# Kernel optimization log

Measured on AMD Instinct MI355X. Metric: run time of the kernel, lower is better.

## Reference

```python
import jax, jax.numpy as jnp
import numpy as np
import math

B, T, C, H = 2, 2048, 1024, 16
HD = C // H  # head_dim = 64
SCALE = 1.0 / math.sqrt(HD)


def _e8_head_dirs(n_heads: int) -> np.ndarray:
    # Type-1 E8 roots in original generation order: (+-1 at i, +-1 at j), i<j,
    # sign order (-1,-1),(-1,1),(1,-1),(1,1); then L2-normalized (norm sqrt(2)).
    roots = []
    for i in range(8):
        for j in range(i + 1, 8):
            for si in (-1.0, 1.0):
                for sj in (-1.0, 1.0):
                    r = np.zeros(8, dtype=np.float32)
                    r[i] = si
                    r[j] = sj
                    roots.append(r)
    roots = np.stack(roots)  # [112, 8], first n_heads used
    roots = roots / np.linalg.norm(roots, axis=1, keepdims=True)
    return roots[:n_heads]


def setup_inputs() -> dict:
    key = jax.random.key(0)
    k1, k2, k3, k4 = jax.random.split(key, 4)
    x = jax.random.normal(k1, (B, T, C), dtype=jnp.float32)
    # nn.Linear-style init scale
    w_qkv = jax.random.normal(k2, (C, 3 * C), dtype=jnp.float32) * (1.0 / math.sqrt(C))
    w_out = jax.random.normal(k3, (C, C), dtype=jnp.float32) * (1.0 / math.sqrt(C))
    head_scales = jax.random.normal(k4, (H,), dtype=jnp.float32) * 0.1
    head_dirs = jnp.asarray(_e8_head_dirs(H))  # [H, 8] buffer (not trained)
    return {"x": x, "w_qkv": w_qkv, "w_out": w_out,
            "head_scales": head_scales, "head_dirs": head_dirs}


def reference(x, w_qkv, w_out, head_scales, head_dirs):
    Bx, Tx, Cx = x.shape
    qkv = (x @ w_qkv).reshape(Bx, Tx, 3, H, HD)
    qkv = jnp.transpose(qkv, (2, 0, 3, 1, 4))  # [3, B, H, T, HD]
    q, k, v = qkv[0], qkv[1], qkv[2]
    scores = jnp.einsum('bhqd,bhkd->bhqk', q, k) * SCALE  # [B,H,T,T]
    causal = jnp.tril(jnp.ones((Tx, Tx), dtype=bool))
    scores = jnp.where(causal[None, None], scores, -jnp.inf)
    # E8 geometric bias: rank-1 per-head bias from projections onto root dirs
    q_proj = jnp.einsum('bhtd,hd->bht', q[..., :8], head_dirs)
    k_proj = jnp.einsum('bhtd,hd->bht', k[..., :8], head_dirs)
    geo_bias = q_proj[..., :, None] * k_proj[..., None, :]  # [B,H,T,T]
    scores = scores + head_scales[None, :, None, None] * geo_bias
    attn = jax.nn.softmax(scores, axis=-1)
    out = jnp.einsum('bhqk,bhkd->bhqd', attn, v)  # [B,H,T,HD]
    out = jnp.transpose(out, (0, 2, 1, 3)).reshape(Bx, Tx, Cx)
    return out @ w_out
```

## Files before the change

kernel.cpp:

```cpp
#include <hip/hip_runtime.h>
#include <stdint.h>


typedef float f32x4 __attribute__((ext_vector_type(4)));
typedef unsigned short u16x8 __attribute__((ext_vector_type(8)));
typedef unsigned short u16x4 __attribute__((ext_vector_type(4)));
typedef unsigned int u32x2 __attribute__((ext_vector_type(2)));
typedef __bf16 bf16x8 __attribute__((ext_vector_type(8)));

static __device__ __forceinline__ unsigned short f2bf(float f) {
  unsigned u = __float_as_uint(f);
  u += 0x7FFFu + ((u >> 16) & 1u);
  return (unsigned short)(u >> 16);
}
static __device__ __forceinline__ float bf2f(unsigned short s) {
  return __uint_as_float(((unsigned)s) << 16);
}
static __device__ __forceinline__ f32x4 mfma16(u16x8 a, u16x8 b, f32x4 c) {
  return __builtin_amdgcn_mfma_f32_16x16x32_bf16(
      __builtin_bit_cast(bf16x8, a), __builtin_bit_cast(bf16x8, b), c, 0, 0, 0);
}
static __device__ __forceinline__ unsigned cvtpk(float lo, float hi) {
  unsigned d;
  asm("v_cvt_pk_bf16_f32 %0, %1, %2" : "=v"(d) : "v"(lo), "v"(hi));
  return d;
}

#define GLD16(gp, lp) __builtin_amdgcn_global_load_lds( \
    (const __attribute__((address_space(1))) unsigned int*)(gp), \
    (__attribute__((address_space(3))) unsigned int*)(lp), 16, 0, 0)

__global__ __launch_bounds__(256) void k_prep(const float* __restrict__ x,
                                              const float* __restrict__ wqkv,
                                              const float* __restrict__ wout,
                                              unsigned short* __restrict__ xb,
                                              unsigned short* __restrict__ wqkvT,
                                              unsigned short* __restrict__ woutT) {
  __shared__ float t[64][65];
  const int bid = blockIdx.x;
  if (bid < 4096) {
    int i = bid * 256 + threadIdx.x;
    f32x4 v = *(const f32x4*)(x + (size_t)i * 4);
    u16x4 o;
#pragma unroll
    for (int j = 0; j < 4; ++j) o[j] = f2bf(v[j]);
    *(u16x4*)(xb + (size_t)i * 4) = o;
    return;
  }
  const float* in;
  unsigned short* out;
  int Cc, bx, by;
  if (bid < 4864) {
    int tt = bid - 4096;
    in = wqkv; out = wqkvT; Cc = 3072;
    bx = tt % 48; by = tt / 48;
  } else {
    int tt = bid - 4864;
    in = wout; out = woutT; Cc = 1024;
    bx = tt & 15; by = tt >> 4;
  }
  const int R = 1024;
  int tr = by * 64, tc = bx * 64;
  int tx = threadIdx.x & 15, ty = threadIdx.x >> 4;
#pragma unroll
  for (int i = 0; i < 4; ++i) {
    int rr = ty + i * 16;
    f32x4 v = *(const f32x4*)(in + (size_t)(tr + rr) * Cc + tc + tx * 4);
#pragma unroll
    for (int j = 0; j < 4; ++j) t[rr][tx * 4 + j] = v[j];
  }
  __syncthreads();
#pragma unroll
  for (int i = 0; i < 4; ++i) {
    int cc = ty + i * 16;
    int rr = tx * 4;
    u16x4 o;
#pragma unroll
    for (int j = 0; j < 4; ++j) o[j] = f2bf(t[rr + j][cc]);
    *(u16x4*)(out + (size_t)(tc + cc) * R + tr + rr) = o;
  }
}

template <int MODE>
__global__ __launch_bounds__(256) void k_gemm(const unsigned short* __restrict__ A,
                                              const unsigned short* __restrict__ Bt,
                                              unsigned short* __restrict__ qo,
                                              unsigned short* __restrict__ ko,
                                              unsigned short* __restrict__ vTo,
                                              float* __restrict__ fo) {
  __shared__ unsigned short lA[128 * 32];
  __shared__ unsigned short lB[128 * 32];
  const int tid = threadIdx.x;
  const int lane = tid & 63, wid = tid >> 6;
  const int wr = wid >> 1, wc = wid & 1;
  const int r = lane & 15, g = lane >> 4;
  const int mbase = blockIdx.y * 128;
  const int nbase = blockIdx.x * 128;

  f32x4 acc[4][4] = {};

  for (int kt = 0; kt < 32; ++kt) {
    __syncthreads();
#pragma unroll
    for (int p = 0; p < 2; ++p) {
      int L = p * 4096 + tid * 16;
      int row = L >> 6;
      int blk = (L >> 4) & 3;
      GLD16(A + (size_t)(mbase + row) * 1024 + kt * 32 + blk * 8, lA + (L >> 1));
      GLD16(Bt + (size_t)(nbase + row) * 1024 + kt * 32 + blk * 8, lB + (L >> 1));
    }
    __syncthreads();
    u16x8 af[4], bfv[4];
#pragma unroll
    for (int m = 0; m < 4; ++m)
      af[m] = *(const u16x8*)(lA + (wr * 64 + m * 16 + r) * 32 + g * 8);
#pragma unroll
    for (int n = 0; n < 4; ++n)
      bfv[n] = *(const u16x8*)(lB + (wc * 64 + n * 16 + r) * 32 + g * 8);
#pragma unroll
    for (int m = 0; m < 4; ++m)
#pragma unroll
      for (int n = 0; n < 4; ++n) acc[m][n] = mfma16(af[m], bfv[n], acc[m][n]);
  }

#pragma unroll
  for (int m = 0; m < 4; ++m) {
#pragma unroll
    for (int n = 0; n < 4; ++n) {
      int ng = nbase + wc * 64 + n * 16 + r;
      int m0 = mbase + wr * 64 + m * 16 + g * 4;
      if (MODE == 0) {
        int sec = ng >> 10, rem = ng & 1023, hh = rem >> 6, d = rem & 63;
        int b = m0 >> 11, t0 = m0 & 2047;
        size_t bh = (size_t)(b * 16 + hh);
        if (sec == 2) {
          u16x4 o;
#pragma unroll
          for (int e = 0; e < 4; ++e) o[e] = f2bf(acc[m][n][e]);
          *(u16x4*)(vTo + (bh * 64 + d) * 2048 + t0) = o;
        } else {
          unsigned short* dst = (sec == 0 ? qo : ko);
#pragma unroll
          for (int e = 0; e < 4; ++e)
            dst[(bh * 2048 + t0 + e) * 64 + d] = f2bf(acc[m][n][e]);
        }
      } else {
#pragma unroll
        for (int e = 0; e < 4; ++e)
          fo[(size_t)(m0 + e) * 1024 + ng] = acc[m][n][e];
      }
    }
  }
}

__global__ __launch_bounds__(256) void k_attn(const unsigned short* __restrict__ qb,
                                              const unsigned short* __restrict__ kb,
                                              const unsigned short* __restrict__ vTb,
                                              const float* __restrict__ hsc,
                                              const float* __restrict__ hdir,
                                              unsigned short* __restrict__ o2) {
  __shared__ unsigned short lK[2][64 * 64];
  __shared__ unsigned short lV[2][64 * 64];
  __shared__ unsigned short lP[4][16 * 64];

  const int tid = threadIdx.x, lane = tid & 63, wid = tid >> 6;
  const int r = lane & 15, g = lane >> 4;
  const int bid = blockIdx.x;
  const int u = bid & 255, kq = bid >> 8;
  const int bh = u & 31, j = u >> 5;
  const int a = (kq == 0) ? j : (kq == 1) ? (31 - j) : (kq == 2) ? (8 + j) : (23 - j);
  const int nk = a + 1;
  const int qbase = a * 64;
  const int h = bh & 15, bi = bh >> 4;

  const size_t kbase = (size_t)bh * (2048 * 64);
  const size_t vbase = (size_t)bh * (64 * 2048);

  auto STAGE = [&](int buf, int kt) {
    unsigned short* dK = (unsigned short*)lK[buf];
    unsigned short* dV = (unsigned short*)lV[buf];
#pragma unroll
    for (int p = 0; p < 2; ++p) {
      int L = p * 4096 + tid * 16;
      int row = L >> 7;
      int cb = (L >> 4) & 7;
      int cbg = cb ^ (row & 7);
      GLD16(kb + kbase + (size_t)(kt * 64 + row) * 64 + cbg * 8, dK + (L >> 1));
      GLD16(vTb + vbase + (size_t)row * 2048 + kt * 64 + cbg * 8, dV + (L >> 1));
    }
  };

  STAGE(0, 0);

  const float LOG2E = 1.44269504088896f;
  const float hs = hsc[h];
  float dir8[8];
#pragma unroll
  for (int j2 = 0; j2 < 8; ++j2) dir8[j2] = hdir[h * 8 + j2];

  u16x8 qc0, qc1;
  {
    const unsigned short* qrow = qb + ((size_t)bh * 2048 + qbase + wid * 16 + r) * 64;
    float proj = 0.f;
    u16x8 qv = *(const u16x8*)qrow;
#pragma unroll
    for (int j2 = 0; j2 < 8; ++j2) proj += bf2f(qv[j2]) * dir8[j2];
#pragma unroll
    for (int s = 0; s < 2; ++s) {
      u16x8 raw = *(const u16x8*)(qrow + s * 32 + g * 8);
      u16x8 ov;
#pragma unroll
      for (int j2 = 0; j2 < 8; ++j2) {
        float v = bf2f(raw[j2]) * (0.125f * LOG2E);
        if (s == 0 && g == 0) v += (hs * LOG2E) * proj * dir8[j2];
        ov[j2] = f2bf(v);
      }
      if (s == 0) qc0 = ov; else qc1 = ov;
    }
  }

  f32x4 accO[4] = {};
  float lp = 0.f;
  unsigned short* pw = &lP[wid][0];
  const int swz = (r & 7) << 4;
  const int qq = qbase + wid * 16 + r;

  asm volatile("s_waitcnt vmcnt(0)" ::: "memory");
  __builtin_amdgcn_sched_barrier(0);
  __builtin_amdgcn_s_barrier();

  for (int kt = 0; kt < nk; ++kt) {
    if (kt + 1 < nk) STAGE((kt + 1) & 1, kt + 1);

    const char* lKc = (const char*)lK[kt & 1];
    const char* lVc = (const char*)lV[kt & 1];

    f32x4 accS[4];
    __builtin_amdgcn_s_setprio(1);
#pragma unroll
    for (int ct = 0; ct < 4; ++ct) {
      f32x4 s4 = {0.f, 0.f, 0.f, 0.f};
      int krow = ct * 16 + r;
      int sw = (krow & 7) << 4;
      u16x8 kf0 = *(const u16x8*)(lKc + krow * 128 + ((g * 16) ^ sw));
      u16x8 kf1 = *(const u16x8*)(lKc + krow * 128 + ((64 + g * 16) ^ sw));
      s4 = mfma16(kf0, qc0, s4);
      s4 = mfma16(kf1, qc1, s4);
      accS[ct] = s4;
    }
    __builtin_amdgcn_s_setprio(0);

    if (kt == nk - 1) {
#pragma unroll
      for (int ct = 0; ct < 4; ++ct)
#pragma unroll
        for (int e = 0; e < 4; ++e) {
          int kk = kt * 64 + ct * 16 + g * 4 + e;
          if (kk > qq) accS[ct][e] = -1e30f;
        }
    }

    float p[4][4];
#pragma unroll
    for (int ct = 0; ct < 4; ++ct)
#pragma unroll
      for (int e = 0; e < 4; ++e) p[ct][e] = exp2f(accS[ct][e]);
#pragma unroll
    for (int ct = 0; ct < 4; ++ct)
      lp += (p[ct][0] + p[ct][1]) + (p[ct][2] + p[ct][3]);

#pragma unroll
    for (int ct = 0; ct < 4; ++ct) {
      u32x2 w;
      w[0] = cvtpk(p[ct][0], p[ct][1]);
      w[1] = cvtpk(p[ct][2], p[ct][3]);
      *(u32x2*)((char*)pw + r * 128 + ((ct * 32 + g * 8) ^ swz)) = w;
    }
    asm volatile("s_waitcnt lgkmcnt(0)" ::: "memory");
    __builtin_amdgcn_sched_barrier(0);

    __builtin_amdgcn_s_setprio(1);
#pragma unroll
    for (int s = 0; s < 2; ++s) {
      u16x8 pa = *(const u16x8*)((const char*)pw + r * 128 + ((s * 64 + g * 16) ^ swz));
#pragma unroll
      for (int dt = 0; dt < 4; ++dt) {
        int dd = dt * 16 + r;
        u16x8 vf = *(const u16x8*)(lVc + dd * 128 + ((s * 64 + g * 16) ^ ((dd & 7) << 4)));
        accO[dt] = mfma16(vf, pa, accO[dt]);
      }
    }
    __builtin_amdgcn_s_setprio(0);

    if (kt + 1 < nk) {
      asm volatile("s_waitcnt vmcnt(0)" ::: "memory");
      __builtin_amdgcn_sched_barrier(0);
      __builtin_amdgcn_s_barrier();
    }
  }

  lp += __shfl_xor(lp, 16, 64);
  lp += __shfl_xor(lp, 32, 64);
  float inv = 1.f / lp;
#pragma unroll
  for (int dt = 0; dt < 4; ++dt) {
    u16x4 o;
#pragma unroll
    for (int e = 0; e < 4; ++e) o[e] = f2bf(accO[dt][e] * inv);
    *(u16x4*)(o2 + ((size_t)(bi * 2048 + qq)) * 1024 + h * 64 + dt * 16 + g * 4) = o;
  }
}

extern "C" void kernel_launch(void* const* d_in, const int* in_sizes, int n_in,
                              void* d_out, int out_size, void* d_ws, size_t ws_size,
                              hipStream_t stream) {
  const float* x    = (const float*)d_in[0];
  const float* wqkv = (const float*)d_in[1];
  const float* wout = (const float*)d_in[2];
  const float* hsc  = (const float*)d_in[3];
  const float* hdir = (const float*)d_in[4];
  float* outp = (float*)d_out;

  char* ws = (char*)d_ws;
  unsigned short* xb    = (unsigned short*)(ws + 0);
  unsigned short* wqkvT = (unsigned short*)(ws + 8388608);
  unsigned short* woutT = (unsigned short*)(ws + 14680064);
  unsigned short* qb    = (unsigned short*)(ws + 16777216);
  unsigned short* kb    = (unsigned short*)(ws + 25165824);
  unsigned short* vT    = (unsigned short*)(ws + 33554432);
  unsigned short* x2b   = (unsigned short*)(ws + 41943040);
  if (ws_size < 50331648u) return;

  k_prep<<<5120, 256, 0, stream>>>(x, wqkv, wout, xb, wqkvT, woutT);
  k_gemm<0><<<dim3(24, 32), 256, 0, stream>>>(xb, wqkvT, qb, kb, vT, nullptr);
  k_attn<<<dim3(1024), 256, 0, stream>>>(qb, kb, vT, hsc, hdir, x2b);
  k_gemm<1><<<dim3(8, 32), 256, 0, stream>>>(x2b, woutT, nullptr, nullptr, nullptr, outp);
}
```

Measured before the change: 111.2 us.

## Pair causal query tiles per block and split key tile across wave halves

The attention kernel now launches 512-thread blocks. Each block handles two query tiles, a short one and its mirrored long one (pr and 31-pr), so every block does exactly 33 key-tile iterations. Within a block, two groups of four waves each take half of each 64-key tile, and their partial outputs and row sums are merged through LDS at the diagonal tile. This balances the causal workload and halves the per-wave MFMA work per key tile. In exchange it adds a cross-wave reduction with an extra barrier and higher register and LDS pressure.

```diff
diff --git a/kernel.cpp b/kernel.cpp
--- a/kernel.cpp
+++ b/kernel.cpp
@@ -153,41 +153,39 @@
   }
 }
 
-__global__ __launch_bounds__(256) void k_attn(const unsigned short* __restrict__ qb,
-                                              const unsigned short* __restrict__ kb,
-                                              const unsigned short* __restrict__ vTb,
-                                              const float* __restrict__ hsc,
-                                              const float* __restrict__ hdir,
-                                              unsigned short* __restrict__ o2) {
+__global__ __launch_bounds__(512, 4) void k_attn(const unsigned short* __restrict__ qb,
+                                                 const unsigned short* __restrict__ kb,
+                                                 const unsigned short* __restrict__ vTb,
+                                                 const float* __restrict__ hsc,
+                                                 const float* __restrict__ hdir,
+                                                 unsigned short* __restrict__ o2) {
   __shared__ unsigned short lK[2][64 * 64];
   __shared__ unsigned short lV[2][64 * 64];
-  __shared__ unsigned short lP[4][16 * 64];
+  __shared__ unsigned short lP[8][16 * 64];
+  __shared__ float lL[128];
 
   const int tid = threadIdx.x, lane = tid & 63, wid = tid >> 6;
   const int r = lane & 15, g = lane >> 4;
+  const int qw = wid & 3, kh = wid >> 2;
   const int bid = blockIdx.x;
-  const int u = bid & 255, kq = bid >> 8;
-  const int bh = u & 31, j = u >> 5;
-  const int a = (kq == 0) ? j : (kq == 1) ? (31 - j) : (kq == 2) ? (8 + j) : (23 - j);
-  const int nk = a + 1;
-  const int qbase = a * 64;
+  const int bh = bid & 31;
+  const int pr = bid >> 5;
+  const int tA = pr, tB = 31 - pr;
+  const int nkA = pr + 1;
   const int h = bh & 15, bi = bh >> 4;
 
   const size_t kbase = (size_t)bh * (2048 * 64);
   const size_t vbase = (size_t)bh * (64 * 2048);
 
   auto STAGE = [&](int buf, int kt) {
-    unsigned short* dK = (unsigned short*)lK[buf];
-    unsigned short* dV = (unsigned short*)lV[buf];
-#pragma unroll
-    for (int p = 0; p < 2; ++p) {
-      int L = p * 4096 + tid * 16;
-      int row = L >> 7;
-      int cb = (L >> 4) & 7;
-      int cbg = cb ^ (row & 7);
-      GLD16(kb + kbase + (size_t)(kt * 64 + row) * 64 + cbg * 8, dK + (L >> 1));
-      GLD16(vTb + vbase + (size_t)row * 2048 + kt * 64 + cbg * 8, dV + (L >> 1));
-    }
+    int L = tid * 16;
+    int row = L >> 7;
+    int cb = (L >> 4) & 7;
+    int cbg = cb ^ (row & 7);
+    GLD16(kb + kbase + (size_t)(kt * 64 + row) * 64 + cbg * 8,
+          (unsigned short*)lK[buf] + (L >> 1));
+    GLD16(vTb + vbase + (size_t)row * 2048 + kt * 64 + cbg * 8,
+          (unsigned short*)lV[buf] + (L >> 1));
   };
 
   STAGE(0, 0);
@@ -198,9 +196,9 @@
 #pragma unroll
   for (int j2 = 0; j2 < 8; ++j2) dir8[j2] = hdir[h * 8 + j2];
 
-  u16x8 qc0, qc1;
-  {
-    const unsigned short* qrow = qb + ((size_t)bh * 2048 + qbase + wid * 16 + r) * 64;
+  u16x8 qAc0, qAc1, qBc0, qBc1;
+  auto QF = [&](int rowbase, u16x8& c0, u16x8& c1) {
+    const unsigned short* qrow = qb + ((size_t)bh * 2048 + rowbase + r) * 64;
     float proj = 0.f;
     u16x8 qv = *(const u16x8*)qrow;
 #pragma unroll
@@ -215,99 +213,126 @@
         if (s == 0 && g == 0) v += (hs * LOG2E) * proj * dir8[j2];
         ov[j2] = f2bf(v);
       }
-      if (s == 0) qc0 = ov; else qc1 = ov;
-    }
-  }
+      if (s == 0) c0 = ov; else c1 = ov;
+    }
+  };
+  QF(tA * 64 + qw * 16, qAc0, qAc1);
+  QF(tB * 64 + qw * 16, qBc0, qBc1);
 
   f32x4 accO[4] = {};
   float lp = 0.f;
+  u16x8 qc0 = qAc0, qc1 = qAc1;
+  int qq = tA * 64 + qw * 16 + r;
   unsigned short* pw = &lP[wid][0];
   const int swz = (r & 7) << 4;
-  const int qq = qbase + wid * 16 + r;
 
   asm volatile("s_waitcnt vmcnt(0)" ::: "memory");
   __builtin_amdgcn_sched_barrier(0);
   __builtin_amdgcn_s_barrier();
 
-  for (int kt = 0; kt < nk; ++kt) {
-    if (kt + 1 < nk) STAGE((kt + 1) & 1, kt + 1);
-
-    const char* lKc = (const char*)lK[kt & 1];
-    const char* lVc = (const char*)lV[kt & 1];
-
-    f32x4 accS[4];
+  for (int it = 0; it < 33; ++it) {
+    if (it + 1 < 33) {
+      int nt = it + 1;
+      STAGE(nt & 1, (nt < nkA) ? nt : nt - nkA);
+    }
+    const int kt = (it < nkA) ? it : it - nkA;
+    const char* lKc = (const char*)lK[it & 1];
+    const char* lVc = (const char*)lV[it & 1];
+
+    f32x4 accS[2];
     __builtin_amdgcn_s_setprio(1);
 #pragma unroll
-    for (int ct = 0; ct < 4; ++ct) {
-      f32x4 s4 = {0.f, 0.f, 0.f, 0.f};
-      int krow = ct * 16 + r;
+    for (int cl = 0; cl < 2; ++cl) {
+      int krow = (kh * 2 + cl) * 16 + r;
       int sw = (krow & 7) << 4;
       u16x8 kf0 = *(const u16x8*)(lKc + krow * 128 + ((g * 16) ^ sw));
       u16x8 kf1 = *(const u16x8*)(lKc + krow * 128 + ((64 + g * 16) ^ sw));
+      f32x4 s4 = {0.f, 0.f, 0.f, 0.f};
       s4 = mfma16(kf0, qc0, s4);
       s4 = mfma16(kf1, qc1, s4);
-      accS[ct] = s4;
+      accS[cl] = s4;
     }
     __builtin_amdgcn_s_setprio(0);
 
-    if (kt == nk - 1) {
-#pragma unroll
-      for (int ct = 0; ct < 4; ++ct)
+    const bool diag = (it == nkA - 1) || (it == 32);
+    if (diag) {
+#pragma unroll
+      for (int cl = 0; cl < 2; ++cl)
 #pragma unroll
         for (int e = 0; e < 4; ++e) {
-          int kk = kt * 64 + ct * 16 + g * 4 + e;
-          if (kk > qq) accS[ct][e] = -1e30f;
+          int kk = kt * 64 + (kh * 2 + cl) * 16 + g * 4 + e;
+          if (kk > qq) accS[cl][e] = -1e30f;
         }
     }
 
-    float p[4][4];
-#pragma unroll
-    for (int ct = 0; ct < 4; ++ct)
-#pragma unroll
-      for (int e = 0; e < 4; ++e) p[ct][e] = exp2f(accS[ct][e]);
-#pragma unroll
-    for (int ct = 0; ct < 4; ++ct)
-      lp += (p[ct][0] + p[ct][1]) + (p[ct][2] + p[ct][3]);
-
-#pragma unroll
-    for (int ct = 0; ct < 4; ++ct) {
+    float p[2][4];
+#pragma unroll
+    for (int cl = 0; cl < 2; ++cl)
+#pragma unroll
+      for (int e = 0; e < 4; ++e) p[cl][e] = exp2f(accS[cl][e]);
+#pragma unroll
+    for (int cl = 0; cl < 2; ++cl)
+      lp += (p[cl][0] + p[cl][1]) + (p[cl][2] + p[cl][3]);
+
+#pragma unroll
+    for (int cl = 0; cl < 2; ++cl) {
       u32x2 w;
-      w[0] = cvtpk(p[ct][0], p[ct][1]);
-      w[1] = cvtpk(p[ct][2], p[ct][3]);
-      *(u32x2*)((char*)pw + r * 128 + ((ct * 32 + g * 8) ^ swz)) = w;
+      w[0] = cvtpk(p[cl][0], p[cl][1]);
+      w[1] = cvtpk(p[cl][2], p[cl][3]);
+      *(u32x2*)((char*)pw + r * 128 + (((kh * 2 + cl) * 32 + g * 8) ^ swz)) = w;
     }
     asm volatile("s_waitcnt lgkmcnt(0)" ::: "memory");
     __builtin_amdgcn_sched_barrier(0);
 
     __builtin_amdgcn_s_setprio(1);
-#pragma unroll
-    for (int s = 0; s < 2; ++s) {
-      u16x8 pa = *(const u16x8*)((const char*)pw + r * 128 + ((s * 64 + g * 16) ^ swz));
+    {
+      u16x8 pa = *(const u16x8*)((const char*)pw + r * 128 + ((kh * 64 + g * 16) ^ swz));
 #pragma unroll
       for (int dt = 0; dt < 4; ++dt) {
         int dd = dt * 16 + r;
-        u16x8 vf = *(const u16x8*)(lVc + dd * 128 + ((s * 64 + g * 16) ^ ((dd & 7) << 4)));
+        u16x8 vf = *(const u16x8*)(lVc + dd * 128 + ((kh * 64 + g * 16) ^ ((dd & 7) << 4)));
         accO[dt] = mfma16(vf, pa, accO[dt]);
       }
     }
     __builtin_amdgcn_s_setprio(0);
 
-    if (kt + 1 < nk) {
+    if (diag) {
+      lp += __shfl_xor(lp, 16, 64);
+      lp += __shfl_xor(lp, 32, 64);
+      char* myR = (char*)&lP[wid][0];
+      const int dtS = kh ? 0 : 2;
+#pragma unroll
+      for (int i = 0; i < 2; ++i)
+        *(f32x4*)(myR + i * 1024 + r * 64 + g * 16) = accO[dtS + i];
+      if (g == 0) lL[wid * 16 + r] = lp;
+      asm volatile("s_waitcnt lgkmcnt(0)" ::: "memory");
+      __builtin_amdgcn_sched_barrier(0);
+      __builtin_amdgcn_s_barrier();
+      const char* pR = (const char*)&lP[wid ^ 4][0];
+      float inv = 1.f / (lp + lL[(wid ^ 4) * 16 + r]);
+      const int dtF = kh ? 2 : 0;
+#pragma unroll
+      for (int i = 0; i < 2; ++i) {
+        f32x4 op = *(const f32x4*)(pR + i * 1024 + r * 64 + g * 16);
+        u16x4 o;
+#pragma unroll
+        for (int e = 0; e < 4; ++e) o[e] = f2bf((accO[dtF + i][e] + op[e]) * inv);
+        *(u16x4*)(o2 + ((size_t)(bi * 2048 + qq)) * 1024 + h * 64 + (dtF + i) * 16 + g * 4) = o;
+      }
+      if (it == nkA - 1 && it != 32) {
+#pragma unroll
+        for (int dt = 0; dt < 4; ++dt) accO[dt] = (f32x4){0.f, 0.f, 0.f, 0.f};
+        lp = 0.f;
+        qq = tB * 64 + qw * 16 + r;
+        qc0 = qBc0; qc1 = qBc1;
+      }
+    }
+
+    if (it + 1 < 33) {
       asm volatile("s_waitcnt vmcnt(0)" ::: "memory");
       __builtin_amdgcn_sched_barrier(0);
       __builtin_amdgcn_s_barrier();
     }
-  }
-
-  lp += __shfl_xor(lp, 16, 64);
-  lp += __shfl_xor(lp, 32, 64);
-  float inv = 1.f / lp;
-#pragma unroll
-  for (int dt = 0; dt < 4; ++dt) {
-    u16x4 o;
-#pragma unroll
-    for (int e = 0; e < 4; ++e) o[e] = f2bf(accO[dt][e] * inv);
-    *(u16x4*)(o2 + ((size_t)(bi * 2048 + qq)) * 1024 + h * 64 + dt * 16 + g * 4) = o;
   }
 }
 
@@ -333,6 +358,6 @@
 
   k_prep<<<5120, 256, 0, stream>>>(x, wqkv, wout, xb, wqkvT, woutT);
   k_gemm<0><<<dim3(24, 32), 256, 0, stream>>>(xb, wqkvT, qb, kb, vT, nullptr);
-  k_attn<<<dim3(1024), 256, 0, stream>>>(qb, kb, vT, hsc, hdir, x2b);
+  k_attn<<<dim3(512), 512, 0, stream>>>(qb, kb, vT, hsc, hdir, x2b);
   k_gemm<1><<<dim3(8, 32), 256, 0, stream>>>(x2b, woutT, nullptr, nullptr, nullptr, outp);
 }
```

After: 117.6 us. +5.8%, slower.
